# Kernel optimization log

Measured on AMD Instinct MI355X. Metric: run time of the kernel, lower is better.

## Reference

```python
import jax, jax.numpy as jnp
import numpy as np

N, E, D, H, ED, L, G = 20000, 320000, 256, 256, 64, 4, 64


def setup_inputs() -> dict:
    key = jax.random.key(0)
    ks = jax.random.split(key, 24)
    w = lambda k, shape: jax.random.normal(k, shape, dtype=jnp.float32) * 0.05
    inp = {
        "x": jax.random.normal(ks[0], (N, D), dtype=jnp.float32),
        "edge_attr": jax.random.normal(ks[1], (E, ED), dtype=jnp.float32),
        "pos": jax.random.normal(ks[2], (N, 3), dtype=jnp.float32),
        "edge_index": jax.random.randint(ks[3], (2, E), 0, N, dtype=jnp.int32),
        "batch": jnp.sort(jax.random.randint(ks[4], (N,), 0, G, dtype=jnp.int32)),
        # stacked per-layer params [L, ...]
        "node_w": w(ks[5], (L, D, H)), "node_b": w(ks[6], (L, H)),
        "edge_w": w(ks[7], (L, ED, H)), "edge_b": w(ks[8], (L, H)),
        "msg_w1": w(ks[9], (L, 2 * H + 1, H)), "msg_b1": w(ks[10], (L, H)),
        "msg_w2": w(ks[11], (L, H, H)), "msg_b2": w(ks[12], (L, H)),
        "upd_w1": w(ks[13], (L, H, H)), "upd_b1": w(ks[14], (L, H)),
        "upd_w2": w(ks[15], (L, H, D)), "upd_b2": w(ks[16], (L, D)),
        # global pooling head
        "fc_w1": w(ks[17], (D, H)), "fc_b1": w(ks[18], (H,)),
        "fc_w2": w(ks[19], (H, 1)), "fc_b2": w(ks[20], (1,)),
    }
    return inp


def reference(x, edge_attr, pos, edge_index, batch,
              node_w, node_b, edge_w, edge_b,
              msg_w1, msg_b1, msg_w2, msg_b2,
              upd_w1, upd_b1, upd_w2, upd_b2,
              fc_w1, fc_b1, fc_w2, fc_b2):
    src = edge_index[0]  # x_j (source / message sender)
    dst = edge_index[1]  # x_i (target / aggregation index)
    # edge distance depends only on fixed pos/edge_index: compute once
    edge_dist = jnp.linalg.norm(pos[src] - pos[dst], axis=1, keepdims=True)  # [E,1]
    silu = jax.nn.silu
    for l in range(L):
        x_emb = x @ node_w[l] + node_b[l]                    # [N,H]
        e_emb = edge_attr @ edge_w[l] + edge_b[l]            # [E,H]
        m_in = jnp.concatenate([x_emb[dst], x_emb[src], edge_dist], axis=-1)  # [E,2H+1]
        m = silu(m_in @ msg_w1[l] + msg_b1[l])
        m = silu(m @ msg_w2[l] + msg_b2[l]) + e_emb          # [E,H]
        aggr = jax.ops.segment_sum(m, dst, num_segments=N)   # scatter-add into target nodes
        x = silu(aggr @ upd_w1[l] + upd_b1[l]) @ upd_w2[l] + upd_b2[l]  # [N,D]
    pooled = jax.ops.segment_sum(x, batch, num_segments=G)   # [G,D]
    out = silu(pooled @ fc_w1 + fc_b1) @ fc_w2 + fc_b2       # [G,1]
    return out
```

## Files before the change

### kernel.cpp

```cpp
#include <hip/hip_runtime.h>
#include <hip/hip_bf16.h>
#include <math.h>

#define N_NODES 20000
#define N_EDGES 320000
#define NGRAPH 64

typedef __attribute__((ext_vector_type(8))) short short8;
typedef __attribute__((ext_vector_type(4))) short short4x;
typedef __attribute__((ext_vector_type(4))) float f32x4;

__device__ __forceinline__ float silu_f(float v){ return v / (1.0f + __expf(-v)); }
__device__ __forceinline__ float bf2f(short s){
  unsigned u = ((unsigned)(unsigned short)s) << 16;
  float f; __builtin_memcpy(&f, &u, 4); return f;
}
__device__ __forceinline__ short f2bf(float f){
  unsigned u; __builtin_memcpy(&u, &f, 4);
  unsigned r = (u + 0x7FFFu + ((u >> 16) & 1u)) >> 16;
  return (short)r;
}

__global__ void k_hist(const int* __restrict__ ei, int* __restrict__ cnt){
  int e = blockIdx.x*256 + threadIdx.x;
  if (e >= N_EDGES) return;
  atomicAdd(&cnt[ei[N_EDGES + e]], 1);
}

__global__ void k_scan(const int* __restrict__ cnt, int* __restrict__ row_ptr,
                       int* __restrict__ off){
  __shared__ int ssum[256];
  int t = threadIdx.x;
  const int CHK = (N_NODES + 255)/256;
  int base = t*CHK;
  int s = 0;
  for(int i=0;i<CHK;i++){ int idx=base+i; if(idx<N_NODES) s += cnt[idx]; }
  ssum[t]=s; __syncthreads();
  for(int o=1;o<256;o<<=1){
    int v = (t>=o)? ssum[t-o] : 0;
    __syncthreads();
    ssum[t] += v;
    __syncthreads();
  }
  int pre = (t==0)? 0 : ssum[t-1];
  for(int i=0;i<CHK;i++){
    int idx=base+i; if(idx>=N_NODES) break;
    row_ptr[idx]=pre; off[idx]=pre; pre += cnt[idx];
  }
  if(t==255) row_ptr[N_NODES]=pre;
}

__global__ void k_scatter(const int* __restrict__ ei, int* __restrict__ off,
                          int* __restrict__ src_s, int* __restrict__ dst_s,
                          int* __restrict__ eid_s){
  int e = blockIdx.x*256 + threadIdx.x;
  if (e >= N_EDGES) return;
  int d = ei[N_EDGES + e];
  int p = atomicAdd(&off[d], 1);
  dst_s[p]=d; src_s[p]=ei[e]; eid_s[p]=e;
}

__global__ void k_dist_s(const int* __restrict__ src_s, const int* __restrict__ dst_s,
                         const float* __restrict__ pos, float* __restrict__ dist_s){
  int i = blockIdx.x*256 + threadIdx.x;
  if (i >= N_EDGES) return;
  int s = src_s[i], d = dst_s[i];
  float dx = pos[s*3+0]-pos[d*3+0];
  float dy = pos[s*3+1]-pos[d*3+1];
  float dz = pos[s*3+2]-pos[d*3+2];
  dist_s[i] = sqrtf(dx*dx+dy*dy+dz*dz);
}

__global__ void k_eaagg_s(const int* __restrict__ row_ptr, const int* __restrict__ eid_s,
                          const float* __restrict__ edge_attr, float* __restrict__ EA){
  int sub = threadIdx.x>>6, j = threadIdx.x&63;
  int d = blockIdx.x*4 + sub;
  if (d >= N_NODES) return;
  int b = row_ptr[d], e = row_ptr[d+1];
  float s = 0.f;
  for(int i=b;i<e;i++) s += edge_attr[(size_t)eid_s[i]*64 + j];
  EA[(size_t)d*96 + j] = s;
  if (j < 32) EA[(size_t)d*96 + 64 + j] = (j==0) ? (float)(e-b) : 0.f;
}

__global__ void k_f2b(const float* __restrict__ S, short* __restrict__ D, int n4){
  int i = blockIdx.x*256 + threadIdx.x;
  if (i >= n4) return;
  float4 v = ((const float4*)S)[i];
  short4x o;
  o[0]=f2bf(v.x); o[1]=f2bf(v.y); o[2]=f2bf(v.z); o[3]=f2bf(v.w);
  ((short4x*)D)[i] = o;
}

__global__ void k_transW(const float* __restrict__ msg_w1, const float* __restrict__ msg_w2,
                         const float* __restrict__ upd_w1, const float* __restrict__ upd_w2,
                         short* __restrict__ wT){
  int z = blockIdx.z; int l = z/5, w = z%5;
  const float* S;
  switch(w){
    case 0: S = msg_w1 + (size_t)l*513*256; break;
    case 1: S = msg_w1 + (size_t)l*513*256 + 256*256; break;
    case 2: S = msg_w2 + (size_t)l*256*256; break;
    case 3: S = upd_w1 + (size_t)l*256*256; break;
    default: S = upd_w2 + (size_t)l*256*256; break;
  }
  short* D = wT + (size_t)z*65536;
  __shared__ float t[32][33];
  int bx = blockIdx.x*32, by = blockIdx.y*32;
  int lx = threadIdx.x & 31, ly = threadIdx.x >> 5;
  #pragma unroll
  for(int r=0;r<4;r++){ int k = ly + r*8; t[k][lx] = S[(size_t)(by+k)*256 + bx+lx]; }
  __syncthreads();
  #pragma unroll
  for(int r=0;r<4;r++){
    int n = ly + r*8;
    D[(size_t)(bx+n)*256 + by+lx] = f2bf(t[lx][n]);
  }
}

__global__ void k_ewaugT(const float* __restrict__ edge_w, const float* __restrict__ edge_b,
                         short* __restrict__ ewT4){
  int n = blockIdx.x, c = threadIdx.x, l = blockIdx.y;
  const float* ew = edge_w + (size_t)l*64*256;
  const float* eb = edge_b + l*256;
  float v = (c < 64) ? ew[(size_t)c*256 + n] : (c == 64 ? eb[n] : 0.f);
  ewT4[(size_t)l*24576 + (size_t)n*96 + c] = f2bf(v);
}

__global__ void k_biasm_acc(const float* __restrict__ node_b, const float* __restrict__ msg_w1,
                            const float* __restrict__ msg_b1, float* __restrict__ biasm4){
  int j = threadIdx.x;
  int b = blockIdx.x, l = blockIdx.y;
  const float* nb  = node_b + l*256;
  const float* w1  = msg_w1 + (size_t)l*513*256;
  float* biasm = biasm4 + l*256;
  if (b == 16){ atomicAdd(&biasm[j], msg_b1[l*256+j]); return; }
  float s = 0.f;
  for(int k = b*16; k < b*16+16; k++)
    s += nb[k]*(w1[(size_t)k*256+j] + w1[(size_t)(256+k)*256+j]);
  atomicAdd(&biasm[j], s);
}

template<int K_REAL, int K_LDS, int AF32, int BIAS, int ACT, int OF32, int OBF16>
__global__ __launch_bounds__(256)
void k_gemm_mfma(const void* __restrict__ A, const short* __restrict__ BT,
                 const float* __restrict__ bias, float* __restrict__ Cf,
                 short* __restrict__ Cb, int M, int Nld,
                 int AzStr, int BzStr, int CzStr){
  __shared__ __align__(16) short As[32][K_LDS];
  const int CHL = K_LDS/8, CH = K_REAL/8;
  int tid = threadIdx.x;
  int zz = blockIdx.z;
  const short* Ab = (const short*)A + (size_t)zz*AzStr;
  const float* Af = (const float*)A + (size_t)zz*AzStr;
  BT += (size_t)zz*BzStr;
  int m0 = blockIdx.y*32, n0 = blockIdx.x*256;
  for(int c = tid; c < 32*CHL; c += 256){
    int row = c / CHL, ch = c % CHL;
    short8 v;
    if (ch < CH) {
      if (AF32){
        float4 f0 = *(const float4*)&Af[(size_t)(m0+row)*K_REAL + ch*8];
        float4 f1 = *(const float4*)&Af[(size_t)(m0+row)*K_REAL + ch*8 + 4];
        v[0]=f2bf(f0.x); v[1]=f2bf(f0.y); v[2]=f2bf(f0.z); v[3]=f2bf(f0.w);
        v[4]=f2bf(f1.x); v[5]=f2bf(f1.y); v[6]=f2bf(f1.z); v[7]=f2bf(f1.w);
      } else {
        v = *(const short8*)&Ab[(size_t)(m0+row)*K_REAL + ch*8];
      }
    } else {
      v = (short8){0,0,0,0,0,0,0,0};
    }
    *(short8*)&As[row][(ch ^ (row&7))*8] = v;
  }
  __syncthreads();
  int wid = tid>>6, lane = tid&63, l15 = lane&15, lq = lane>>4;
  int ncol0 = n0 + wid*64;
  f32x4 acc[2][4];
  #pragma unroll
  for(int mt=0;mt<2;mt++)
    #pragma unroll
    for(int nt=0;nt<4;nt++) acc[mt][nt] = (f32x4){0.f,0.f,0.f,0.f};
  for(int k0=0;k0<K_REAL;k0+=32){
    int kc = k0 + 8*lq;
    short8 a[2], b[4];
    #pragma unroll
    for(int mt=0;mt<2;mt++){
      int row = mt*16 + l15;
      a[mt] = *(const short8*)&As[row][kc ^ ((row&7)<<3)];
    }
    #pragma unroll
    for(int nt=0;nt<4;nt++){
      int col = ncol0 + nt*16 + l15;
      b[nt] = *(const short8*)&BT[(size_t)col*K_REAL + kc];
    }
    #pragma unroll
    for(int mt=0;mt<2;mt++)
      #pragma unroll
      for(int nt=0;nt<4;nt++)
        acc[mt][nt] = __builtin_amdgcn_mfma_f32_16x16x32_bf16(a[mt], b[nt], acc[mt][nt], 0, 0, 0);
  }
  #pragma unroll
  for(int mt=0;mt<2;mt++){
    #pragma unroll
    for(int nt=0;nt<4;nt++){
      int col = ncol0 + nt*16 + l15;
      float bb = BIAS ? bias[col] : 0.f;
      #pragma unroll
      for(int r=0;r<4;r++){
        int row = m0 + mt*16 + lq*4 + r;
        float v = acc[mt][nt][r] + bb;
        if (ACT) v = silu_f(v);
        if (OF32)  Cf[(size_t)zz*CzStr + (size_t)row*Nld + col] = v;
        if (OBF16) Cb[(size_t)zz*CzStr + (size_t)row*Nld + col] = f2bf(v);
      }
    }
  }
}

__global__ __launch_bounds__(256)
void k_edge_mfma(const short* __restrict__ t_ab,
                 const float* __restrict__ dist_s,
                 const int* __restrict__ src_s, const int* __restrict__ dst_s,
                 const float* __restrict__ w1c, const float* __restrict__ biasm,
                 const short* __restrict__ w2T, const float* __restrict__ b2,
                 float* __restrict__ aggr)
{
  __shared__ __align__(16) unsigned char ulds[256*17*4];
  short (*h)[256] = (short(*)[256])ulds;
  float* outl = (float*)ulds;
  __shared__ int sdst[32], ssrc[32];
  __shared__ float sdist[32];
  int tid = threadIdx.x;
  int e0 = blockIdx.x*32;
  if (tid < 32){
    sdst[tid] = dst_s[e0 + tid];
    ssrc[tid] = src_s[e0 + tid];
    sdist[tid] = dist_s[e0 + tid];
  }
  __syncthreads();
  int wid = tid>>6, lane = tid&63;
  int half = lane>>5, cl = lane&31;
  float wc8[8], bm8[8];
  {
    float4 w0 = *(const float4*)&w1c[8*cl], w1v = *(const float4*)&w1c[8*cl+4];
    float4 b0 = *(const float4*)&biasm[8*cl], b1v = *(const float4*)&biasm[8*cl+4];
    wc8[0]=w0.x; wc8[1]=w0.y; wc8[2]=w0.z; wc8[3]=w0.w;
    wc8[4]=w1v.x; wc8[5]=w1v.y; wc8[6]=w1v.z; wc8[7]=w1v.w;
    bm8[0]=b0.x; bm8[1]=b0.y; bm8[2]=b0.z; bm8[3]=b0.w;
    bm8[4]=b1v.x; bm8[5]=b1v.y; bm8[6]=b1v.z; bm8[7]=b1v.w;
  }
  int ebase = wid*8 + half*4;
  int dprev = -1;
  short8 va;
  #pragma unroll
  for(int p=0;p<4;p++){
    int e = ebase + p;
    int d = sdst[e], s = ssrc[e];
    if (d != dprev){
      va = *(const short8*)&t_ab[(size_t)d*512 + 8*cl];
      dprev = d;
    }
    short8 vb = *(const short8*)&t_ab[(size_t)s*512 + 256 + 8*cl];
    float de = sdist[e];
    short8 hv;
    #pragma unroll
    for(int i=0;i<8;i++){
      float f = bf2f(va[i]) + bf2f(vb[i]) + de*wc8[i] + bm8[i];
      hv[i] = f2bf(silu_f(f));
    }
    *(short8*)&h[e][(8*cl) ^ ((e&7)<<3)] = hv;
  }
  __syncthreads();

  int l15 = lane & 15, lq = lane >> 4;
  int nb = wid*64;
  f32x4 acc[2][4];
  #pragma unroll
  for(int mt=0;mt<2;mt++)
    #pragma unroll
    for(int nt=0;nt<4;nt++) acc[mt][nt] = (f32x4){0.f,0.f,0.f,0.f};

  for(int k0=0;k0<256;k0+=32){
    int kc = k0 + 8*lq;
    short8 a[2], b[4];
    #pragma unroll
    for(int mt=0;mt<2;mt++){
      int row = mt*16 + l15;
      a[mt] = *(const short8*)&h[row][kc ^ ((row&7)<<3)];
    }
    #pragma unroll
    for(int nt=0;nt<4;nt++){
      int col = nb + nt*16 + l15;
      b[nt] = *(const short8*)&w2T[(size_t)col*256 + kc];
    }
    #pragma unroll
    for(int mt=0;mt<2;mt++)
      #pragma unroll
      for(int nt=0;nt<4;nt++)
        acc[mt][nt] = __builtin_amdgcn_mfma_f32_16x16x32_bf16(a[mt], b[nt], acc[mt][nt], 0, 0, 0);
  }
  __syncthreads();

  int j = tid;
  float accu = 0.f;
  int prev = sdst[0];
  #pragma unroll
  for(int mt=0;mt<2;mt++){
    #pragma unroll
    for(int nt=0;nt<4;nt++){
      int col = nb + nt*16 + l15;
      float bb = b2[col];
      #pragma unroll
      for(int r=0;r<4;r++){
        int row = lq*4 + r;
        outl[col*17 + row] = silu_f(acc[mt][nt][r] + bb);
      }
    }
    __syncthreads();
    #pragma unroll
    for(int e2=0;e2<16;e2++){
      int d = sdst[mt*16 + e2];
      if (d != prev){
        atomicAdd(&aggr[(size_t)prev*256 + j], accu);
        accu = 0.f; prev = d;
      }
      accu += outl[j*17 + e2];
    }
    __syncthreads();
  }
  atomicAdd(&aggr[(size_t)prev*256 + j], accu);
}

__global__ void k_ghist(const int* __restrict__ batch, int* __restrict__ gcnt){
  int n = blockIdx.x*256 + threadIdx.x;
  if (n >= N_NODES) return;
  atomicAdd(&gcnt[batch[n]], 1);
}
__global__ void k_gscan(const int* __restrict__ gcnt, int* __restrict__ gptr){
  if (threadIdx.x == 0){
    int s = 0;
    for(int g=0; g<NGRAPH; g++){ gptr[g]=s; s += gcnt[g]; }
    gptr[NGRAPH] = s;
  }
}
__global__ void k_pool_seg(const float* __restrict__ x, const int* __restrict__ gptr,
                           float* __restrict__ pooled){
  int g = blockIdx.x, j = threadIdx.x;
  int b = gptr[g], e = gptr[g+1];
  float s = 0.f;
  for(int n=b; n<e; n++) s += x[(size_t)n*256 + j];
  pooled[g*256 + j] = s;
}

__global__ void k_head(const float* __restrict__ pooled, const float* __restrict__ fw1,
                       const float* __restrict__ fb1, const float* __restrict__ fw2,
                       const float* __restrict__ fb2, float* __restrict__ out){
  __shared__ float red[256];
  int g = blockIdx.x, j = threadIdx.x;
  float s = fb1[j];
  const float* p = &pooled[g*256];
  for(int k=0;k<256;k++) s += p[k]*fw1[k*256+j];
  float hv = silu_f(s)*fw2[j];
  red[j]=hv; __syncthreads();
  for(int off=128;off>0;off>>=1){ if(j<off) red[j]+=red[j+off]; __syncthreads(); }
  if(j==0) out[g] = red[0] + fb2[0];
}

extern "C" void kernel_launch(void* const* d_in, const int* in_sizes, int n_in,
                              void* d_out, int out_size, void* d_ws, size_t ws_size,
                              hipStream_t stream) {
  const float* x_in      = (const float*)d_in[0];
  const float* edge_attr = (const float*)d_in[1];
  const float* pos       = (const float*)d_in[2];
  const int*   ei        = (const int*)d_in[3];
  const int*   batch     = (const int*)d_in[4];
  const float* node_w    = (const float*)d_in[5];
  const float* node_b    = (const float*)d_in[6];
  const float* edge_w    = (const float*)d_in[7];
  const float* edge_b    = (const float*)d_in[8];
  const float* msg_w1    = (const float*)d_in[9];
  const float* msg_b1    = (const float*)d_in[10];
  const float* msg_w2    = (const float*)d_in[11];
  const float* msg_b2    = (const float*)d_in[12];
  const float* upd_w1    = (const float*)d_in[13];
  const float* upd_b1    = (const float*)d_in[14];
  const float* upd_w2    = (const float*)d_in[15];
  const float* upd_b2    = (const float*)d_in[16];
  const float* fc_w1     = (const float*)d_in[17];
  const float* fc_b1     = (const float*)d_in[18];
  const float* fc_w2     = (const float*)d_in[19];
  const float* fc_b2     = (const float*)d_in[20];
  float* out = (float*)d_out;

  float* ws = (float*)d_ws;
  int* cnt     = (int*)ws; ws += N_NODES;
  int* off     = (int*)ws; ws += N_NODES;
  int* row_ptr = (int*)ws; ws += N_NODES+4;
  int* src_s   = (int*)ws; ws += N_EDGES;
  int* dst_s   = (int*)ws; ws += N_EDGES;
  int* eid_s   = (int*)ws; ws += N_EDGES;
  float* dist_s= ws; ws += N_EDGES;
  int* gcnt    = (int*)ws; ws += NGRAPH;
  int* gptr    = (int*)ws; ws += NGRAPH+4;
  short* wT     = (short*)ws; ws += 20*65536/2;
  short* nw_bf4 = (short*)ws; ws += 4*65536/2;
  short* ewT4   = (short*)ws; ws += 4*24576/2;
  short* WabT4  = (short*)ws; ws += 4*131072/2;
  float* biasm4 = ws; ws += 4*256;
  short* x_bf   = (short*)ws; ws += (size_t)N_NODES*256/2;
  float* EA_aug = ws; ws += (size_t)N_NODES*96;
  float* tabreg = ws; ws += (size_t)N_NODES*256;
  float* aggr   = ws; ws += (size_t)N_NODES*256;
  float* pooled = ws; ws += NGRAPH*256;

  short* t_ab   = (short*)tabreg;
  short* h_bf   = (short*)tabreg;
  float* xfinal = aggr;

  hipMemsetAsync(cnt, 0, N_NODES*sizeof(int), stream);
  k_hist<<<(N_EDGES+255)/256, 256, 0, stream>>>(ei, cnt);
  k_scan<<<1, 256, 0, stream>>>(cnt, row_ptr, off);
  k_scatter<<<(N_EDGES+255)/256, 256, 0, stream>>>(ei, off, src_s, dst_s, eid_s);
  k_dist_s<<<(N_EDGES+255)/256, 256, 0, stream>>>(src_s, dst_s, pos, dist_s);
  k_eaagg_s<<<N_NODES/4, 256, 0, stream>>>(row_ptr, eid_s, edge_attr, EA_aug);
  hipMemsetAsync(gcnt, 0, NGRAPH*sizeof(int), stream);
  k_ghist<<<(N_NODES+255)/256, 256, 0, stream>>>(batch, gcnt);
  k_gscan<<<1, 64, 0, stream>>>(gcnt, gptr);

  k_transW<<<dim3(8,8,20), 256, 0, stream>>>(msg_w1, msg_w2, upd_w1, upd_w2, wT);
  k_ewaugT<<<dim3(256,4), 96, 0, stream>>>(edge_w, edge_b, ewT4);
  k_f2b<<<256, 256, 0, stream>>>(node_w, nw_bf4, 4*65536/4);
  hipMemsetAsync(biasm4, 0, 4*256*sizeof(float), stream);
  k_biasm_acc<<<dim3(17,4), 256, 0, stream>>>(node_b, msg_w1, msg_b1, biasm4);
  k_gemm_mfma<256,256,0,0,0,0,1><<<dim3(1,8,4), 256, 0, stream>>>(
      wT,          nw_bf4, nullptr, nullptr, WabT4,         256, 256, 5*65536, 65536, 131072);
  k_gemm_mfma<256,256,0,0,0,0,1><<<dim3(1,8,4), 256, 0, stream>>>(
      wT + 65536,  nw_bf4, nullptr, nullptr, WabT4 + 65536, 256, 256, 5*65536, 65536, 131072);

  for(int l=0;l<4;l++){
    const float* w1  = msg_w1 + (size_t)l*513*256;
    const float* mb2 = msg_b2 + l*256;
    const float* ub1 = upd_b1 + l*256;
    const float* ub2 = upd_b2 + l*256;
    const short* w2T_l  = wT + (size_t)(l*5+2)*65536;
    const short* uw1T_l = wT + (size_t)(l*5+3)*65536;
    const short* uw2T_l = wT + (size_t)(l*5+4)*65536;

    if (l == 0)
      k_gemm_mfma<256,256,1,0,0,0,1><<<dim3(2,625), 256, 0, stream>>>(
          x_in, WabT4 + (size_t)l*131072, nullptr, nullptr, t_ab, N_NODES, 512, 0,0,0);
    else
      k_gemm_mfma<256,256,0,0,0,0,1><<<dim3(2,625), 256, 0, stream>>>(
          x_bf, WabT4 + (size_t)l*131072, nullptr, nullptr, t_ab, N_NODES, 512, 0,0,0);

    k_gemm_mfma<96,128,1,0,0,1,0><<<dim3(1,625), 256, 0, stream>>>(
        EA_aug, ewT4 + (size_t)l*24576, nullptr, aggr, nullptr, N_NODES, 256, 0,0,0);

    k_edge_mfma<<<N_EDGES/32, 256, 0, stream>>>(t_ab, dist_s, src_s, dst_s,
                                                w1 + 512*256, biasm4 + l*256,
                                                w2T_l, mb2, aggr);

    k_gemm_mfma<256,256,1,1,1,0,1><<<dim3(1,625), 256, 0, stream>>>(
        aggr, uw1T_l, ub1, nullptr, h_bf, N_NODES, 256, 0,0,0);
    if (l < 3)
      k_gemm_mfma<256,256,0,1,0,0,1><<<dim3(1,625), 256, 0, stream>>>(
          h_bf, uw2T_l, ub2, nullptr, x_bf, N_NODES, 256, 0,0,0);
    else
      k_gemm_mfma<256,256,0,1,0,1,0><<<dim3(1,625), 256, 0, stream>>>(
          h_bf, uw2T_l, ub2, xfinal, nullptr, N_NODES, 256, 0,0,0);
  }

  k_pool_seg<<<NGRAPH, 256, 0, stream>>>(xfinal, gptr, pooled);
  k_head<<<NGRAPH, 256, 0, stream>>>(pooled, fc_w1, fc_b1, fc_w2, fc_b2, out);
}
```

Before: 1.399 ms.

## Fold update output weight into next layer's node projection; widen edge tile

For layers 0-2 the upd_w2 GEMM and the next layer's node projection GEMM are fused algebraically. The product upd_w2 × Wab is precomputed once, and upd_b2 is folded into the message bias, so each layer does one 256→512 GEMM straight from h instead of two GEMMs plus an x round trip. This removes one N×256×256 GEMM and an intermediate write/read per layer. The edge kernel also now handles 64 edges per block instead of 32, which reuses the w2T B-fragments across twice as many rows and drops the consecutive-dst reuse of the t_ab row load. The fold adds extra bf16 rounding of the combined weight.

```diff
diff --git a/kernel.cpp b/kernel.cpp
--- a/kernel.cpp
+++ b/kernel.cpp
@@ -139,6 +139,18 @@
   for(int k = b*16; k < b*16+16; k++)
     s += nb[k]*(w1[(size_t)k*256+j] + w1[(size_t)(256+k)*256+j]);
   atomicAdd(&biasm[j], s);
+}
+
+__global__ void k_biasfold(const float* __restrict__ upd_b2, const short* __restrict__ WabT4,
+                           float* __restrict__ biasm4){
+  int l = blockIdx.x + 1;
+  int j = threadIdx.x;
+  const float* ub2 = upd_b2 + (size_t)(l-1)*256;
+  const short* W = WabT4 + (size_t)l*131072;
+  float s = 0.f;
+  for(int k=0;k<256;k++)
+    s += ub2[k]*(bf2f(W[(size_t)j*256+k]) + bf2f(W[(size_t)(256+j)*256+k]));
+  biasm4[l*256 + j] += s;
 }
 
 template<int K_REAL, int K_LDS, int AF32, int BIAS, int ACT, int OF32, int OBF16>
@@ -225,21 +237,20 @@
                  const short* __restrict__ w2T, const float* __restrict__ b2,
                  float* __restrict__ aggr)
 {
-  __shared__ __align__(16) unsigned char ulds[256*17*4];
+  __shared__ __align__(16) unsigned char ulds[256*33*4];
   short (*h)[256] = (short(*)[256])ulds;
   float* outl = (float*)ulds;
-  __shared__ int sdst[32], ssrc[32];
-  __shared__ float sdist[32];
+  __shared__ int sdst[64], ssrc[64];
+  __shared__ float sdist[64];
   int tid = threadIdx.x;
-  int e0 = blockIdx.x*32;
-  if (tid < 32){
+  int e0 = blockIdx.x*64;
+  if (tid < 64){
     sdst[tid] = dst_s[e0 + tid];
     ssrc[tid] = src_s[e0 + tid];
     sdist[tid] = dist_s[e0 + tid];
   }
   __syncthreads();
-  int wid = tid>>6, lane = tid&63;
-  int half = lane>>5, cl = lane&31;
+  int cl = tid & 31, slot = tid >> 5;
   float wc8[8], bm8[8];
   {
     float4 w0 = *(const float4*)&w1c[8*cl], w1v = *(const float4*)&w1c[8*cl+4];
@@ -249,19 +260,13 @@
     bm8[0]=b0.x; bm8[1]=b0.y; bm8[2]=b0.z; bm8[3]=b0.w;
     bm8[4]=b1v.x; bm8[5]=b1v.y; bm8[6]=b1v.z; bm8[7]=b1v.w;
   }
-  int ebase = wid*8 + half*4;
-  int dprev = -1;
-  short8 va;
-  #pragma unroll
-  for(int p=0;p<4;p++){
-    int e = ebase + p;
+  #pragma unroll
+  for(int p=0;p<8;p++){
+    int e = slot + p*8;
     int d = sdst[e], s = ssrc[e];
-    if (d != dprev){
-      va = *(const short8*)&t_ab[(size_t)d*512 + 8*cl];
-      dprev = d;
-    }
+    float de = sdist[e];
+    short8 va = *(const short8*)&t_ab[(size_t)d*512 + 8*cl];
     short8 vb = *(const short8*)&t_ab[(size_t)s*512 + 256 + 8*cl];
-    float de = sdist[e];
     short8 hv;
     #pragma unroll
     for(int i=0;i<8;i++){
@@ -272,32 +277,39 @@
   }
   __syncthreads();
 
-  int l15 = lane & 15, lq = lane >> 4;
+  int wid = tid>>6, lane = tid&63, l15 = lane&15, lq = lane>>4;
   int nb = wid*64;
-  f32x4 acc[2][4];
-  #pragma unroll
-  for(int mt=0;mt<2;mt++)
-    #pragma unroll
-    for(int nt=0;nt<4;nt++) acc[mt][nt] = (f32x4){0.f,0.f,0.f,0.f};
+  f32x4 acc[2][2][4];
+  #pragma unroll
+  for(int s=0;s<2;s++)
+    #pragma unroll
+    for(int mt=0;mt<2;mt++)
+      #pragma unroll
+      for(int nt=0;nt<4;nt++) acc[s][mt][nt] = (f32x4){0.f,0.f,0.f,0.f};
 
   for(int k0=0;k0<256;k0+=32){
     int kc = k0 + 8*lq;
-    short8 a[2], b[4];
-    #pragma unroll
-    for(int mt=0;mt<2;mt++){
-      int row = mt*16 + l15;
-      a[mt] = *(const short8*)&h[row][kc ^ ((row&7)<<3)];
-    }
+    short8 b[4];
     #pragma unroll
     for(int nt=0;nt<4;nt++){
       int col = nb + nt*16 + l15;
       b[nt] = *(const short8*)&w2T[(size_t)col*256 + kc];
     }
-    #pragma unroll
-    for(int mt=0;mt<2;mt++)
-      #pragma unroll
-      for(int nt=0;nt<4;nt++)
-        acc[mt][nt] = __builtin_amdgcn_mfma_f32_16x16x32_bf16(a[mt], b[nt], acc[mt][nt], 0, 0, 0);
+    short8 a[2][2];
+    #pragma unroll
+    for(int s=0;s<2;s++)
+      #pragma unroll
+      for(int mt=0;mt<2;mt++){
+        int row = s*32 + mt*16 + l15;
+        a[s][mt] = *(const short8*)&h[row][kc ^ ((row&7)<<3)];
+      }
+    #pragma unroll
+    for(int s=0;s<2;s++)
+      #pragma unroll
+      for(int mt=0;mt<2;mt++)
+        #pragma unroll
+        for(int nt=0;nt<4;nt++)
+          acc[s][mt][nt] = __builtin_amdgcn_mfma_f32_16x16x32_bf16(a[s][mt], b[nt], acc[s][mt][nt], 0, 0, 0);
   }
   __syncthreads();
 
@@ -305,26 +317,29 @@
   float accu = 0.f;
   int prev = sdst[0];
   #pragma unroll
-  for(int mt=0;mt<2;mt++){
-    #pragma unroll
-    for(int nt=0;nt<4;nt++){
-      int col = nb + nt*16 + l15;
-      float bb = b2[col];
-      #pragma unroll
-      for(int r=0;r<4;r++){
-        int row = lq*4 + r;
-        outl[col*17 + row] = silu_f(acc[mt][nt][r] + bb);
+  for(int s=0;s<2;s++){
+    #pragma unroll
+    for(int mt=0;mt<2;mt++){
+      #pragma unroll
+      for(int nt=0;nt<4;nt++){
+        int col = nb + nt*16 + l15;
+        float bb = b2[col];
+        #pragma unroll
+        for(int r=0;r<4;r++){
+          int row = mt*16 + lq*4 + r;
+          outl[col*33 + row] = silu_f(acc[s][mt][nt][r] + bb);
+        }
       }
     }
     __syncthreads();
     #pragma unroll
-    for(int e2=0;e2<16;e2++){
-      int d = sdst[mt*16 + e2];
+    for(int e2=0;e2<32;e2++){
+      int d = sdst[s*32 + e2];
       if (d != prev){
         atomicAdd(&aggr[(size_t)prev*256 + j], accu);
         accu = 0.f; prev = d;
       }
-      accu += outl[j*17 + e2];
+      accu += outl[j*33 + e2];
     }
     __syncthreads();
   }
@@ -402,19 +417,20 @@
   float* dist_s= ws; ws += N_EDGES;
   int* gcnt    = (int*)ws; ws += NGRAPH;
   int* gptr    = (int*)ws; ws += NGRAPH+4;
-  short* wT     = (short*)ws; ws += 20*65536/2;
-  short* nw_bf4 = (short*)ws; ws += 4*65536/2;
-  short* ewT4   = (short*)ws; ws += 4*24576/2;
-  short* WabT4  = (short*)ws; ws += 4*131072/2;
-  float* biasm4 = ws; ws += 4*256;
-  short* x_bf   = (short*)ws; ws += (size_t)N_NODES*256/2;
+  short* wT      = (short*)ws; ws += 20*65536/2;
+  short* nw_bf4  = (short*)ws; ws += 4*65536/2;
+  short* uw2_bf4 = (short*)ws; ws += 4*65536/2;
+  short* ewT4    = (short*)ws; ws += 4*24576/2;
+  short* WabT4   = (short*)ws; ws += 4*131072/2;
+  short* WfoldT4 = (short*)ws; ws += 3*131072/2;
+  float* biasm4  = ws; ws += 4*256;
+  short* h_bf   = (short*)ws; ws += (size_t)N_NODES*256/2;
   float* EA_aug = ws; ws += (size_t)N_NODES*96;
   float* tabreg = ws; ws += (size_t)N_NODES*256;
   float* aggr   = ws; ws += (size_t)N_NODES*256;
   float* pooled = ws; ws += NGRAPH*256;
 
   short* t_ab   = (short*)tabreg;
-  short* h_bf   = (short*)tabreg;
   float* xfinal = aggr;
 
   hipMemsetAsync(cnt, 0, N_NODES*sizeof(int), stream);
@@ -430,12 +446,19 @@
   k_transW<<<dim3(8,8,20), 256, 0, stream>>>(msg_w1, msg_w2, upd_w1, upd_w2, wT);
   k_ewaugT<<<dim3(256,4), 96, 0, stream>>>(edge_w, edge_b, ewT4);
   k_f2b<<<256, 256, 0, stream>>>(node_w, nw_bf4, 4*65536/4);
+  k_f2b<<<256, 256, 0, stream>>>(upd_w2, uw2_bf4, 4*65536/4);
   hipMemsetAsync(biasm4, 0, 4*256*sizeof(float), stream);
   k_biasm_acc<<<dim3(17,4), 256, 0, stream>>>(node_b, msg_w1, msg_b1, biasm4);
   k_gemm_mfma<256,256,0,0,0,0,1><<<dim3(1,8,4), 256, 0, stream>>>(
       wT,          nw_bf4, nullptr, nullptr, WabT4,         256, 256, 5*65536, 65536, 131072);
   k_gemm_mfma<256,256,0,0,0,0,1><<<dim3(1,8,4), 256, 0, stream>>>(
       wT + 65536,  nw_bf4, nullptr, nullptr, WabT4 + 65536, 256, 256, 5*65536, 65536, 131072);
+  k_gemm_mfma<256,256,0,0,0,0,1><<<dim3(1,16,3), 256, 0, stream>>>(
+      WabT4 + 131072, uw2_bf4, nullptr, nullptr, WfoldT4, 512, 256, 131072, 65536, 131072);
+  k_biasfold<<<3, 256, 0, stream>>>(upd_b2, WabT4, biasm4);
+
+  k_gemm_mfma<256,256,1,0,0,0,1><<<dim3(2,625), 256, 0, stream>>>(
+      x_in, WabT4, nullptr, nullptr, t_ab, N_NODES, 512, 0,0,0);
 
   for(int l=0;l<4;l++){
     const float* w1  = msg_w1 + (size_t)l*513*256;
@@ -446,25 +469,19 @@
     const short* uw1T_l = wT + (size_t)(l*5+3)*65536;
     const short* uw2T_l = wT + (size_t)(l*5+4)*65536;
 
-    if (l == 0)
-      k_gemm_mfma<256,256,1,0,0,0,1><<<dim3(2,625), 256, 0, stream>>>(
-          x_in, WabT4 + (size_t)l*131072, nullptr, nullptr, t_ab, N_NODES, 512, 0,0,0);
-    else
-      k_gemm_mfma<256,256,0,0,0,0,1><<<dim3(2,625), 256, 0, stream>>>(
-          x_bf, WabT4 + (size_t)l*131072, nullptr, nullptr, t_ab, N_NODES, 512, 0,0,0);
-
     k_gemm_mfma<96,128,1,0,0,1,0><<<dim3(1,625), 256, 0, stream>>>(
         EA_aug, ewT4 + (size_t)l*24576, nullptr, aggr, nullptr, N_NODES, 256, 0,0,0);
 
-    k_edge_mfma<<<N_EDGES/32, 256, 0, stream>>>(t_ab, dist_s, src_s, dst_s,
+    k_edge_mfma<<<N_EDGES/64, 256, 0, stream>>>(t_ab, dist_s, src_s, dst_s,
                                                 w1 + 512*256, biasm4 + l*256,
                                                 w2T_l, mb2, aggr);
 
     k_gemm_mfma<256,256,1,1,1,0,1><<<dim3(1,625), 256, 0, stream>>>(
         aggr, uw1T_l, ub1, nullptr, h_bf, N_NODES, 256, 0,0,0);
+
     if (l < 3)
-      k_gemm_mfma<256,256,0,1,0,0,1><<<dim3(1,625), 256, 0, stream>>>(
-          h_bf, uw2T_l, ub2, nullptr, x_bf, N_NODES, 256, 0,0,0);
+      k_gemm_mfma<256,256,0,0,0,0,1><<<dim3(2,625), 256, 0, stream>>>(
+          h_bf, WfoldT4 + (size_t)l*131072, nullptr, nullptr, t_ab, N_NODES, 512, 0,0,0);
     else
       k_gemm_mfma<256,256,0,1,0,1,0><<<dim3(1,625), 256, 0, stream>>>(
           h_bf, uw2T_l, ub2, xfinal, nullptr, N_NODES, 256, 0,0,0);
```

Measured after the change: 1.323 ms. -5.4%, faster.

## Fold edge embedding into update GEMM and fuse upd_w2 with next layer projection

Applied to the files above, without the earlier changes.

Folds the per-node aggregated edge-embedding term into an extended upd_w1 GEMM (K=352) so the separate edge GEMM is removed, and aggr is zeroed with a memset. For layers 0-2 it precomputes upd_w2 times the next layer's node/message weights, so one GEMM goes straight from h to t_ab, with the bias folded into biasm. The edge kernel now stages its output in bf16 in LDS and does one 32-edge segmented reduction. In exchange it adds extra bf16 rounding of the folded weights and of the message outputs before aggregation.

```diff
diff --git a/kernel.cpp b/kernel.cpp
--- a/kernel.cpp
+++ b/kernel.cpp
@@ -118,13 +118,24 @@
   }
 }
 
-__global__ void k_ewaugT(const float* __restrict__ edge_w, const float* __restrict__ edge_b,
-                         short* __restrict__ ewT4){
-  int n = blockIdx.x, c = threadIdx.x, l = blockIdx.y;
-  const float* ew = edge_w + (size_t)l*64*256;
-  const float* eb = edge_b + l*256;
-  float v = (c < 64) ? ew[(size_t)c*256 + n] : (c == 64 ? eb[n] : 0.f);
-  ewT4[(size_t)l*24576 + (size_t)n*96 + c] = f2bf(v);
+__global__ void k_uw1ext(const short* __restrict__ wT, const float* __restrict__ edge_w,
+                         const float* __restrict__ edge_b, short* __restrict__ uw1ext4){
+  int n = blockIdx.x, l = blockIdx.y, tid = threadIdx.x;
+  const short* uw1T = wT + (size_t)(l*5+3)*65536;
+  short* dst = uw1ext4 + (size_t)l*256*352 + (size_t)n*352;
+  dst[tid] = uw1T[(size_t)n*256 + tid];
+  if (tid < 96){
+    int c = tid;
+    float s = 0.f;
+    if (c < 64){
+      const float* er = edge_w + (size_t)l*64*256 + (size_t)c*256;
+      for(int m=0;m<256;m++) s += bf2f(uw1T[(size_t)n*256+m])*er[m];
+    } else if (c == 64){
+      const float* er = edge_b + (size_t)l*256;
+      for(int m=0;m<256;m++) s += bf2f(uw1T[(size_t)n*256+m])*er[m];
+    }
+    dst[256 + c] = f2bf(s);
+  }
 }
 
 __global__ void k_biasm_acc(const float* __restrict__ node_b, const float* __restrict__ msg_w1,
@@ -141,9 +152,22 @@
   atomicAdd(&biasm[j], s);
 }
 
-template<int K_REAL, int K_LDS, int AF32, int BIAS, int ACT, int OF32, int OBF16>
+__global__ void k_biasfold(const float* __restrict__ upd_b2, const short* __restrict__ WabT4,
+                           float* __restrict__ biasm4){
+  int l = blockIdx.x + 1;
+  int j = threadIdx.x;
+  const float* ub2 = upd_b2 + (size_t)(l-1)*256;
+  const short* W = WabT4 + (size_t)l*131072;
+  float s = 0.f;
+  for(int k=0;k<256;k++)
+    s += ub2[k]*(bf2f(W[(size_t)j*256+k]) + bf2f(W[(size_t)(256+j)*256+k]));
+  biasm4[l*256 + j] += s;
+}
+
+template<int K_REAL, int K_LDS, int AF32, int AEXT, int BIAS, int ACT, int OF32, int OBF16>
 __global__ __launch_bounds__(256)
-void k_gemm_mfma(const void* __restrict__ A, const short* __restrict__ BT,
+void k_gemm_mfma(const void* __restrict__ A, const float* __restrict__ A2,
+                 const short* __restrict__ BT,
                  const float* __restrict__ bias, float* __restrict__ Cf,
                  short* __restrict__ Cb, int M, int Nld,
                  int AzStr, int BzStr, int CzStr){
@@ -157,8 +181,20 @@
   int m0 = blockIdx.y*32, n0 = blockIdx.x*256;
   for(int c = tid; c < 32*CHL; c += 256){
     int row = c / CHL, ch = c % CHL;
-    short8 v;
-    if (ch < CH) {
+    short8 v = (short8){0,0,0,0,0,0,0,0};
+    if (AEXT){
+      if (ch < 32){
+        float4 f0 = *(const float4*)&Af[(size_t)(m0+row)*256 + ch*8];
+        float4 f1 = *(const float4*)&Af[(size_t)(m0+row)*256 + ch*8 + 4];
+        v[0]=f2bf(f0.x); v[1]=f2bf(f0.y); v[2]=f2bf(f0.z); v[3]=f2bf(f0.w);
+        v[4]=f2bf(f1.x); v[5]=f2bf(f1.y); v[6]=f2bf(f1.z); v[7]=f2bf(f1.w);
+      } else if (ch < 44){
+        float4 f0 = *(const float4*)&A2[(size_t)(m0+row)*96 + (ch-32)*8];
+        float4 f1 = *(const float4*)&A2[(size_t)(m0+row)*96 + (ch-32)*8 + 4];
+        v[0]=f2bf(f0.x); v[1]=f2bf(f0.y); v[2]=f2bf(f0.z); v[3]=f2bf(f0.w);
+        v[4]=f2bf(f1.x); v[5]=f2bf(f1.y); v[6]=f2bf(f1.z); v[7]=f2bf(f1.w);
+      }
+    } else if (ch < CH) {
       if (AF32){
         float4 f0 = *(const float4*)&Af[(size_t)(m0+row)*K_REAL + ch*8];
         float4 f1 = *(const float4*)&Af[(size_t)(m0+row)*K_REAL + ch*8 + 4];
@@ -167,8 +203,6 @@
       } else {
         v = *(const short8*)&Ab[(size_t)(m0+row)*K_REAL + ch*8];
       }
-    } else {
-      v = (short8){0,0,0,0,0,0,0,0};
     }
     *(short8*)&As[row][(ch ^ (row&7))*8] = v;
   }
@@ -225,9 +259,9 @@
                  const short* __restrict__ w2T, const float* __restrict__ b2,
                  float* __restrict__ aggr)
 {
-  __shared__ __align__(16) unsigned char ulds[256*17*4];
+  __shared__ __align__(16) unsigned char ulds[256*34*2];
   short (*h)[256] = (short(*)[256])ulds;
-  float* outl = (float*)ulds;
+  short* outl = (short*)ulds;
   __shared__ int sdst[32], ssrc[32];
   __shared__ float sdist[32];
   int tid = threadIdx.x;
@@ -249,19 +283,13 @@
     bm8[0]=b0.x; bm8[1]=b0.y; bm8[2]=b0.z; bm8[3]=b0.w;
     bm8[4]=b1v.x; bm8[5]=b1v.y; bm8[6]=b1v.z; bm8[7]=b1v.w;
   }
-  int ebase = wid*8 + half*4;
-  int dprev = -1;
-  short8 va;
   #pragma unroll
   for(int p=0;p<4;p++){
-    int e = ebase + p;
+    int e = wid*8 + p*2 + half;
     int d = sdst[e], s = ssrc[e];
-    if (d != dprev){
-      va = *(const short8*)&t_ab[(size_t)d*512 + 8*cl];
-      dprev = d;
-    }
+    float de = sdist[e];
+    short8 va = *(const short8*)&t_ab[(size_t)d*512 + 8*cl];
     short8 vb = *(const short8*)&t_ab[(size_t)s*512 + 256 + 8*cl];
-    float de = sdist[e];
     short8 hv;
     #pragma unroll
     for(int i=0;i<8;i++){
@@ -301,9 +329,6 @@
   }
   __syncthreads();
 
-  int j = tid;
-  float accu = 0.f;
-  int prev = sdst[0];
   #pragma unroll
   for(int mt=0;mt<2;mt++){
     #pragma unroll
@@ -312,21 +337,24 @@
       float bb = b2[col];
       #pragma unroll
       for(int r=0;r<4;r++){
-        int row = lq*4 + r;
-        outl[col*17 + row] = silu_f(acc[mt][nt][r] + bb);
+        int row = mt*16 + lq*4 + r;
+        outl[col*34 + row] = f2bf(silu_f(acc[mt][nt][r] + bb));
       }
     }
-    __syncthreads();
-    #pragma unroll
-    for(int e2=0;e2<16;e2++){
-      int d = sdst[mt*16 + e2];
-      if (d != prev){
-        atomicAdd(&aggr[(size_t)prev*256 + j], accu);
-        accu = 0.f; prev = d;
-      }
-      accu += outl[j*17 + e2];
-    }
-    __syncthreads();
+  }
+  __syncthreads();
+
+  int j = tid;
+  float accu = 0.f;
+  int prev = sdst[0];
+  #pragma unroll
+  for(int e=0;e<32;e++){
+    int d = sdst[e];
+    if (d != prev){
+      atomicAdd(&aggr[(size_t)prev*256 + j], accu);
+      accu = 0.f; prev = d;
+    }
+    accu += bf2f(outl[j*34 + e]);
   }
   atomicAdd(&aggr[(size_t)prev*256 + j], accu);
 }
@@ -402,19 +430,20 @@
   float* dist_s= ws; ws += N_EDGES;
   int* gcnt    = (int*)ws; ws += NGRAPH;
   int* gptr    = (int*)ws; ws += NGRAPH+4;
-  short* wT     = (short*)ws; ws += 20*65536/2;
-  short* nw_bf4 = (short*)ws; ws += 4*65536/2;
-  short* ewT4   = (short*)ws; ws += 4*24576/2;
-  short* WabT4  = (short*)ws; ws += 4*131072/2;
-  float* biasm4 = ws; ws += 4*256;
-  short* x_bf   = (short*)ws; ws += (size_t)N_NODES*256/2;
+  short* wT      = (short*)ws; ws += 20*65536/2;
+  short* nw_bf4  = (short*)ws; ws += 4*65536/2;
+  short* uw2_bf4 = (short*)ws; ws += 4*65536/2;
+  short* uw1ext4 = (short*)ws; ws += 4*256*352/2 + 64;
+  short* WabT4   = (short*)ws; ws += 4*131072/2;
+  short* WfoldT4 = (short*)ws; ws += 3*131072/2;
+  float* biasm4  = ws; ws += 4*256;
+  short* h_bf   = (short*)ws; ws += (size_t)N_NODES*256/2;
   float* EA_aug = ws; ws += (size_t)N_NODES*96;
   float* tabreg = ws; ws += (size_t)N_NODES*256;
   float* aggr   = ws; ws += (size_t)N_NODES*256;
   float* pooled = ws; ws += NGRAPH*256;
 
   short* t_ab   = (short*)tabreg;
-  short* h_bf   = (short*)tabreg;
   float* xfinal = aggr;
 
   hipMemsetAsync(cnt, 0, N_NODES*sizeof(int), stream);
@@ -428,14 +457,21 @@
   k_gscan<<<1, 64, 0, stream>>>(gcnt, gptr);
 
   k_transW<<<dim3(8,8,20), 256, 0, stream>>>(msg_w1, msg_w2, upd_w1, upd_w2, wT);
-  k_ewaugT<<<dim3(256,4), 96, 0, stream>>>(edge_w, edge_b, ewT4);
   k_f2b<<<256, 256, 0, stream>>>(node_w, nw_bf4, 4*65536/4);
+  k_f2b<<<256, 256, 0, stream>>>(upd_w2, uw2_bf4, 4*65536/4);
+  k_uw1ext<<<dim3(256,4), 256, 0, stream>>>(wT, edge_w, edge_b, uw1ext4);
   hipMemsetAsync(biasm4, 0, 4*256*sizeof(float), stream);
   k_biasm_acc<<<dim3(17,4), 256, 0, stream>>>(node_b, msg_w1, msg_b1, biasm4);
-  k_gemm_mfma<256,256,0,0,0,0,1><<<dim3(1,8,4), 256, 0, stream>>>(
-      wT,          nw_bf4, nullptr, nullptr, WabT4,         256, 256, 5*65536, 65536, 131072);
-  k_gemm_mfma<256,256,0,0,0,0,1><<<dim3(1,8,4), 256, 0, stream>>>(
-      wT + 65536,  nw_bf4, nullptr, nullptr, WabT4 + 65536, 256, 256, 5*65536, 65536, 131072);
+  k_gemm_mfma<256,256,0,0,0,0,0,1><<<dim3(1,8,4), 256, 0, stream>>>(
+      wT,         nullptr, nw_bf4, nullptr, nullptr, WabT4,         256, 256, 5*65536, 65536, 131072);
+  k_gemm_mfma<256,256,0,0,0,0,0,1><<<dim3(1,8,4), 256, 0, stream>>>(
+      wT + 65536, nullptr, nw_bf4, nullptr, nullptr, WabT4 + 65536, 256, 256, 5*65536, 65536, 131072);
+  k_gemm_mfma<256,256,0,0,0,0,0,1><<<dim3(1,16,3), 256, 0, stream>>>(
+      WabT4 + 131072, nullptr, uw2_bf4, nullptr, nullptr, WfoldT4, 512, 256, 131072, 65536, 131072);
+  k_biasfold<<<3, 256, 0, stream>>>(upd_b2, WabT4, biasm4);
+
+  k_gemm_mfma<256,256,1,0,0,0,0,1><<<dim3(2,625), 256, 0, stream>>>(
+      x_in, nullptr, WabT4, nullptr, nullptr, t_ab, N_NODES, 512, 0,0,0);
 
   for(int l=0;l<4;l++){
     const float* w1  = msg_w1 + (size_t)l*513*256;
@@ -443,31 +479,23 @@
     const float* ub1 = upd_b1 + l*256;
     const float* ub2 = upd_b2 + l*256;
     const short* w2T_l  = wT + (size_t)(l*5+2)*65536;
-    const short* uw1T_l = wT + (size_t)(l*5+3)*65536;
     const short* uw2T_l = wT + (size_t)(l*5+4)*65536;
 
-    if (l == 0)
-      k_gemm_mfma<256,256,1,0,0,0,1><<<dim3(2,625), 256, 0, stream>>>(
-          x_in, WabT4 + (size_t)l*131072, nullptr, nullptr, t_ab, N_NODES, 512, 0,0,0);
-    else
-      k_gemm_mfma<256,256,0,0,0,0,1><<<dim3(2,625), 256, 0, stream>>>(
-          x_bf, WabT4 + (size_t)l*131072, nullptr, nullptr, t_ab, N_NODES, 512, 0,0,0);
-
-    k_gemm_mfma<96,128,1,0,0,1,0><<<dim3(1,625), 256, 0, stream>>>(
-        EA_aug, ewT4 + (size_t)l*24576, nullptr, aggr, nullptr, N_NODES, 256, 0,0,0);
+    hipMemsetAsync(aggr, 0, (size_t)N_NODES*256*sizeof(float), stream);
 
     k_edge_mfma<<<N_EDGES/32, 256, 0, stream>>>(t_ab, dist_s, src_s, dst_s,
                                                 w1 + 512*256, biasm4 + l*256,
                                                 w2T_l, mb2, aggr);
 
-    k_gemm_mfma<256,256,1,1,1,0,1><<<dim3(1,625), 256, 0, stream>>>(
-        aggr, uw1T_l, ub1, nullptr, h_bf, N_NODES, 256, 0,0,0);
+    k_gemm_mfma<352,384,1,1,1,1,0,1><<<dim3(1,625), 256, 0, stream>>>(
+        aggr, EA_aug, uw1ext4 + (size_t)l*256*352, ub1, nullptr, h_bf, N_NODES, 256, 0,0,0);
+
     if (l < 3)
-      k_gemm_mfma<256,256,0,1,0,0,1><<<dim3(1,625), 256, 0, stream>>>(
-          h_bf, uw2T_l, ub2, nullptr, x_bf, N_NODES, 256, 0,0,0);
+      k_gemm_mfma<256,256,0,0,0,0,0,1><<<dim3(2,625), 256, 0, stream>>>(
+          h_bf, nullptr, WfoldT4 + (size_t)l*131072, nullptr, nullptr, t_ab, N_NODES, 512, 0,0,0);
     else
-      k_gemm_mfma<256,256,0,1,0,1,0><<<dim3(1,625), 256, 0, stream>>>(
-          h_bf, uw2T_l, ub2, xfinal, nullptr, N_NODES, 256, 0,0,0);
+      k_gemm_mfma<256,256,0,0,1,0,1,0><<<dim3(1,625), 256, 0, stream>>>(
+          h_bf, nullptr, uw2T_l, ub2, xfinal, nullptr, N_NODES, 256, 0,0,0);
   }
 
   k_pool_seg<<<NGRAPH, 256, 0, stream>>>(xfinal, gptr, pooled);
```

New measurement: 1.298 ms. 1.08x faster.
